# Performance work log

Hardware: AMD Instinct MI355X
Metric: run time of the kernel (lower is better)

The kernel has to match this reference:

```python
import jax, jax.numpy as jnp
import numpy as np

NUM_HEADS = 8
HEAD_DIM = 64  # inner_dim 512 / 8 heads
SCALE = HEAD_DIM ** -0.5


def setup_inputs() -> dict:
    key = jax.random.key(0)
    kq, kk, kv, kp = jax.random.split(key, 4)
    B, S, D = 8, 1024, 512
    q = jax.random.normal(kq, (B, S, D), dtype=jnp.float32)
    k = jax.random.normal(kk, (B, S, D), dtype=jnp.float32)
    v = jax.random.normal(kv, (B, S, D), dtype=jnp.float32)
    # learned additive positional bias table (trunc-normal init approximated by normal clipped)
    pos_bias = jnp.clip(jax.random.normal(kp, (1, NUM_HEADS, S, S), dtype=jnp.float32), -2.0, 2.0)
    return {"q": q, "k": k, "v": v, "pos_bias": pos_bias}


def reference(q, k, v, pos_bias):
    B, S, D = q.shape
    h, d = NUM_HEADS, HEAD_DIM
    # b n (h d) -> b h n d
    qh = q.reshape(B, S, h, d).transpose(0, 2, 1, 3) * SCALE
    kh = k.reshape(B, S, h, d).transpose(0, 2, 1, 3)
    vh = v.reshape(B, S, h, d).transpose(0, 2, 1, 3)
    sim = jnp.einsum('bhid,bhjd->bhij', qh, kh) + pos_bias
    attn = jax.nn.softmax(sim, axis=-1)
    out = jnp.einsum('bhij,bhjd->bhid', attn, vh)
    # b h n d -> b n (h d)
    return out.transpose(0, 2, 1, 3).reshape(B, S, h * d)
```

## Files before the change

### kernel.cpp

```cpp
#include <hip/hip_runtime.h>
#include <hip/hip_bf16.h>
#include <hip/hip_fp16.h>
#include <math.h>


typedef __attribute__((ext_vector_type(8))) short short8;
typedef __attribute__((ext_vector_type(4))) float f32x4;
typedef __attribute__((ext_vector_type(4))) unsigned short u16x4;
typedef __attribute__((ext_vector_type(8))) unsigned short u16x8;

#define SEQ   1024
#define DM    512
#define HD    64
#define NH    8
#define LOG2E 1.4426950408889634f
#define QSCALE (0.125f * LOG2E)

__device__ __forceinline__ unsigned short f2bf(float f) {
    unsigned u = __float_as_uint(f);
    u += 0x7fffu + ((u >> 16) & 1u);
    return (unsigned short)(u >> 16);
}
__device__ __forceinline__ u16x4 pack4(float a, float b, float c, float d) {
    u16x4 r; r[0] = f2bf(a); r[1] = f2bf(b); r[2] = f2bf(c); r[3] = f2bf(d);
    return r;
}
__device__ __forceinline__ short8 pack8(const float* x) {
    short8 r;
#pragma unroll
    for (int i = 0; i < 8; ++i) r[i] = (short)f2bf(x[i]);
    return r;
}
__device__ __forceinline__ float fexp2(float x) {
#if __has_builtin(__builtin_amdgcn_exp2f)
    return __builtin_amdgcn_exp2f(x);
#else
    return exp2f(x);
#endif
}
__device__ __forceinline__ void gll16(const void* g, void* l) {
    __builtin_amdgcn_global_load_lds(
        (const __attribute__((address_space(1))) unsigned*)g,
        (__attribute__((address_space(3))) unsigned*)l, 16, 0, 0);
}
__device__ __forceinline__ float h2f(unsigned short u) {
    __half hh = *reinterpret_cast<__half*>(&u);
    return __half2float(hh);
}
__device__ __forceinline__ unsigned short f2h(float v) {
    __half hh = __float2half(v);
    return *reinterpret_cast<unsigned short*>(&hh);
}

__global__ __launch_bounds__(256)
void prep_k(const float* __restrict__ k, short* __restrict__ kws) {
    int tid = blockIdx.x * 256 + threadIdx.x;
    int d8 = tid & 7, h = (tid >> 3) & 7, s = (tid >> 6) & 1023, b = tid >> 16;
    const float* src = k + ((size_t)(b * SEQ + s) * DM + h * HD + d8 * 8);
    float4 x0 = *(const float4*)src, x1 = *(const float4*)(src + 4);
    float xs[8] = {x0.x, x0.y, x0.z, x0.w, x1.x, x1.y, x1.z, x1.w};
    int bh = b * NH + h;
    size_t idx = (size_t)(bh * 16 + (s >> 6)) * 4096 + (s & 63) * 64 + ((d8 ^ (s & 7)) * 8);
    *(short8*)(kws + idx) = pack8(xs);
}

__global__ __launch_bounds__(256)
void prep_v(const float* __restrict__ v, short* __restrict__ vtws) {
    __shared__ short Vs[64][72];
    int bid = blockIdx.x;
    int st = bid & 15, h = (bid >> 4) & 7, b = bid >> 7;
    int t = threadIdx.x;
    {
        int sl = t >> 2, dc = t & 3;
        const float* src = v + ((size_t)(b * SEQ + st * 64 + sl) * DM + h * HD + dc * 16);
        float4 a0 = ((const float4*)src)[0], a1 = ((const float4*)src)[1],
               a2 = ((const float4*)src)[2], a3 = ((const float4*)src)[3];
        float xs0[8] = {a0.x, a0.y, a0.z, a0.w, a1.x, a1.y, a1.z, a1.w};
        float xs1[8] = {a2.x, a2.y, a2.z, a2.w, a3.x, a3.y, a3.z, a3.w};
        *(short8*)&Vs[sl][dc * 16]     = pack8(xs0);
        *(short8*)&Vs[sl][dc * 16 + 8] = pack8(xs1);
    }
    __syncthreads();
    {
        int d = t >> 2, sc = t & 3;
        short vals[16];
#pragma unroll
        for (int j = 0; j < 16; ++j) vals[j] = Vs[sc * 16 + j][d];
        short8 w0, w1;
#pragma unroll
        for (int j = 0; j < 8; ++j) { w0[j] = vals[j]; w1[j] = vals[8 + j]; }
        int bh = b * NH + h;
        size_t base = (size_t)(bh * 16 + st) * 4096 + d * 64;
        int c0 = (sc * 2) ^ (d & 7), c1 = (sc * 2 + 1) ^ (d & 7);
        *(short8*)(vtws + base + c0 * 8) = w0;
        *(short8*)(vtws + base + c1 * 8) = w1;
    }
}

__global__ __launch_bounds__(256)
void prep_bias(const float* __restrict__ bias, unsigned short* __restrict__ b16) {
    int tid = blockIdx.x * 256 + threadIdx.x;
    int h = tid >> 18;
    int rem = tid & 262143;
    int i = rem >> 8;
    int j = (rem & 255) * 4;
    float4 x = *(const float4*)(bias + ((size_t)(h * 1024 + i) * 1024 + j));
    int kt = j >> 6, jl = j & 63, mt = jl >> 4, gg = (jl >> 2) & 3;
    u16x4 r;
    r[0] = f2h(x.x * LOG2E); r[1] = f2h(x.y * LOG2E);
    r[2] = f2h(x.z * LOG2E); r[3] = f2h(x.w * LOG2E);
    *(u16x4*)(b16 + ((size_t)((h * 16 + kt) * 1024 + i) * 64 + gg * 16 + mt * 4)) = r;
}

template<int BM>
__global__ __launch_bounds__(256, 4)
void attn_fwd3(const float* __restrict__ q,
               const float* __restrict__ bias32,
               const unsigned short* __restrict__ bias16,
               const short* __restrict__ kws,
               const short* __restrict__ vtws,
               float* __restrict__ out)
{
    __shared__ short Ksh[2][4096];
    __shared__ short Vsh[2][4096];
    __shared__ short Plds[4][16][64];

    const int t = threadIdx.x;
    const int wid = t >> 6, lane = t & 63;
    const int qr = lane & 15, g = lane >> 4;

    int raw = blockIdx.x;
    int lid = (raw & 7) * 128 + (raw >> 3);
    const int b = lid & 7;
    const int h = (lid >> 3) & 7;
    const int qt = lid >> 6;
    const int qbase = qt * 64 + wid * 16;
    const int bh = b * NH + h;

    const float* qp = q + ((size_t)(b * SEQ + qbase + qr) * DM + h * HD);
    short8 qf[2];
#pragma unroll
    for (int c = 0; c < 2; ++c) {
        float4 x0 = *(const float4*)(qp + g * 8 + 32 * c);
        float4 x1 = *(const float4*)(qp + g * 8 + 32 * c + 4);
        float xs[8] = {x0.x * QSCALE, x0.y * QSCALE, x0.z * QSCALE, x0.w * QSCALE,
                       x1.x * QSCALE, x1.y * QSCALE, x1.z * QSCALE, x1.w * QSCALE};
        qf[c] = pack8(xs);
    }

    f32x4 o[4];
#pragma unroll
    for (int nt = 0; nt < 4; ++nt) o[nt] = (f32x4){0.f, 0.f, 0.f, 0.f};
    float mrun = -INFINITY, lrun = 0.f;

    const size_t tb0 = (size_t)bh * 16 * 4096;

    u16x8 bn0, bn1;
    float4 bnf[4];

    {
        const short* gk = kws + tb0 + wid * 512 + lane * 8;
        const short* gv = vtws + tb0 + wid * 512 + lane * 8;
        gll16(gk,        &Ksh[0][wid * 512]);
        gll16(gk + 2048, &Ksh[0][2048 + wid * 512]);
        gll16(gv,        &Vsh[0][wid * 512]);
        gll16(gv + 2048, &Vsh[0][2048 + wid * 512]);
        if constexpr (BM == 0) {
            const unsigned short* bp =
                bias16 + ((size_t)((h * 16 + 0) * 1024 + qbase + qr) * 64 + g * 16);
            bn0 = *(const u16x8*)bp;
            bn1 = *(const u16x8*)(bp + 8);
        } else {
            const float* bp = bias32 + ((size_t)(h * SEQ + qbase + qr) * SEQ + g * 4);
#pragma unroll
            for (int mt = 0; mt < 4; ++mt) bnf[mt] = *(const float4*)(bp + 16 * mt);
        }
    }
    __syncthreads();

    int cur = 0;
    for (int kt = 0; kt < 16; ++kt) {
        float bf[4][4];
        if constexpr (BM == 0) {
#pragma unroll
            for (int r = 0; r < 4; ++r) {
                bf[0][r] = h2f(bn0[r]);
                bf[1][r] = h2f(bn0[4 + r]);
                bf[2][r] = h2f(bn1[r]);
                bf[3][r] = h2f(bn1[4 + r]);
            }
        } else {
#pragma unroll
            for (int mt = 0; mt < 4; ++mt)
#pragma unroll
                for (int r = 0; r < 4; ++r) bf[mt][r] = ((const float*)&bnf[mt])[r];
        }

        if (kt < 15) {
            const size_t tb = tb0 + (size_t)(kt + 1) * 4096;
            const short* gk = kws + tb + wid * 512 + lane * 8;
            const short* gv = vtws + tb + wid * 512 + lane * 8;
            int nxt = cur ^ 1;
            gll16(gk,        &Ksh[nxt][wid * 512]);
            gll16(gk + 2048, &Ksh[nxt][2048 + wid * 512]);
            gll16(gv,        &Vsh[nxt][wid * 512]);
            gll16(gv + 2048, &Vsh[nxt][2048 + wid * 512]);
        }
        {
            int ktn = kt < 15 ? kt + 1 : 15;
            if constexpr (BM == 0) {
                const unsigned short* bp =
                    bias16 + ((size_t)((h * 16 + ktn) * 1024 + qbase + qr) * 64 + g * 16);
                bn0 = *(const u16x8*)bp;
                bn1 = *(const u16x8*)(bp + 8);
            } else {
                const float* bp =
                    bias32 + ((size_t)(h * SEQ + qbase + qr) * SEQ + ktn * 64 + g * 4);
#pragma unroll
                for (int mt = 0; mt < 4; ++mt) bnf[mt] = *(const float4*)(bp + 16 * mt);
            }
        }

        f32x4 acc[4];
#pragma unroll
        for (int mt = 0; mt < 4; ++mt) acc[mt] = (f32x4){0.f, 0.f, 0.f, 0.f};
        __builtin_amdgcn_s_setprio(1);
#pragma unroll
        for (int mt = 0; mt < 4; ++mt) {
#pragma unroll
            for (int c = 0; c < 2; ++c) {
                const short8 kf = *(const short8*)
                    &Ksh[cur][(qr + 16 * mt) * 64 + ((g + 4 * c) ^ (qr & 7)) * 8];
                acc[mt] = __builtin_amdgcn_mfma_f32_16x16x32_bf16(kf, qf[c], acc[mt], 0, 0, 0);
            }
        }
        __builtin_amdgcn_s_setprio(0);

        float s[4][4];
        float tmax = -INFINITY;
#pragma unroll
        for (int mt = 0; mt < 4; ++mt)
#pragma unroll
            for (int r = 0; r < 4; ++r) {
                float val;
                if constexpr (BM == 0) val = acc[mt][r] + bf[mt][r];
                else                   val = fmaf(bf[mt][r], LOG2E, acc[mt][r]);
                s[mt][r] = val;
                tmax = fmaxf(tmax, val);
            }
        tmax = fmaxf(tmax, __shfl_xor(tmax, 16));
        tmax = fmaxf(tmax, __shfl_xor(tmax, 32));
        const float mnew = fmaxf(mrun, tmax);
        float ssum = 0.f;
#pragma unroll
        for (int mt = 0; mt < 4; ++mt) {
            float e0 = fexp2(s[mt][0] - mnew);
            float e1 = fexp2(s[mt][1] - mnew);
            float e2 = fexp2(s[mt][2] - mnew);
            float e3 = fexp2(s[mt][3] - mnew);
            ssum += (e0 + e1) + (e2 + e3);
            *(u16x4*)&Plds[wid][qr][((4 * mt + g) ^ (2 * (qr & 7))) * 4] =
                pack4(e0, e1, e2, e3);
        }
        ssum += __shfl_xor(ssum, 16);
        ssum += __shfl_xor(ssum, 32);
        const float scs = fexp2(mrun - mnew);
        lrun = lrun * scs + ssum;
        mrun = mnew;

        float scr[4];
#pragma unroll
        for (int r = 0; r < 4; ++r) scr[r] = __shfl(scs, g * 4 + r);
#pragma unroll
        for (int nt = 0; nt < 4; ++nt)
#pragma unroll
            for (int r = 0; r < 4; ++r) o[nt][r] *= scr[r];

        asm volatile("s_waitcnt lgkmcnt(0)" ::: "memory");
        __builtin_amdgcn_sched_barrier(0);

        __builtin_amdgcn_s_setprio(1);
#pragma unroll
        for (int c = 0; c < 2; ++c) {
            const int ch0 = (2 * g + 8 * c) ^ (2 * (qr & 7));
            short8 pf = *(const short8*)&Plds[wid][qr][ch0 * 4];
#pragma unroll
            for (int nt = 0; nt < 4; ++nt) {
                short8 vf = *(const short8*)
                    &Vsh[cur][(qr + 16 * nt) * 64 + ((g + 4 * c) ^ (qr & 7)) * 8];
                o[nt] = __builtin_amdgcn_mfma_f32_16x16x32_bf16(pf, vf, o[nt], 0, 0, 0);
            }
        }
        __builtin_amdgcn_s_setprio(0);

        __syncthreads();
        cur ^= 1;
    }

    const float inv = 1.0f / lrun;
    float invr[4];
#pragma unroll
    for (int r = 0; r < 4; ++r) invr[r] = __shfl(inv, g * 4 + r);
    float* op = out + ((size_t)(b * SEQ + qbase) * DM + h * HD + qr);
#pragma unroll
    for (int nt = 0; nt < 4; ++nt)
#pragma unroll
        for (int r = 0; r < 4; ++r)
            op[(size_t)(g * 4 + r) * DM + nt * 16] = o[nt][r] * invr[r];
}

__global__ __launch_bounds__(256, 3)
void attn_fwd(const float* __restrict__ q, const float* __restrict__ k,
              const float* __restrict__ v, const float* __restrict__ bias,
              float* __restrict__ out)
{
    __shared__ short Klds[64][72];
    __shared__ short Vt[64][72];
    __shared__ short Pl[4][16][72];

    const int t = threadIdx.x;
    const int wid = t >> 6;
    const int lane = t & 63;
    const int qr = lane & 15;
    const int g = lane >> 4;

    int idx = blockIdx.x;
    const int b = idx & 7;  idx >>= 3;
    const int h = idx & 7;
    const int qtile = idx >> 3;
    const int qbase = qtile * 64 + wid * 16;

    const float* qp = q + ((b * SEQ + qbase + qr) * DM + h * HD);
    short8 qf[2];
#pragma unroll
    for (int c = 0; c < 2; ++c) {
        float4 x0 = *reinterpret_cast<const float4*>(qp + g * 8 + 32 * c);
        float4 x1 = *reinterpret_cast<const float4*>(qp + g * 8 + 32 * c + 4);
        float xs[8] = {x0.x * 0.125f, x0.y * 0.125f, x0.z * 0.125f, x0.w * 0.125f,
                       x1.x * 0.125f, x1.y * 0.125f, x1.z * 0.125f, x1.w * 0.125f};
        qf[c] = pack8(xs);
    }

    f32x4 o[4];
#pragma unroll
    for (int nt = 0; nt < 4; ++nt) o[nt] = (f32x4){0.f, 0.f, 0.f, 0.f};
    float mrun = -INFINITY, lrun = 0.f;

    const int jrow = t & 63;
    const int cc = t >> 6;

    for (int kt = 0; kt < 16; ++kt) {
        const int kbase = kt * 64;
        {
            const float4* kp4 = reinterpret_cast<const float4*>(
                k + ((b * SEQ + kbase + jrow) * DM + h * HD + cc * 16));
            float4 a0 = kp4[0], a1 = kp4[1], a2 = kp4[2], a3 = kp4[3];
            u16x4* dst = reinterpret_cast<u16x4*>(&Klds[jrow][cc * 16]);
            dst[0] = pack4(a0.x, a0.y, a0.z, a0.w);
            dst[1] = pack4(a1.x, a1.y, a1.z, a1.w);
            dst[2] = pack4(a2.x, a2.y, a2.z, a2.w);
            dst[3] = pack4(a3.x, a3.y, a3.z, a3.w);
        }
        {
            const float* vp = v + ((b * SEQ + kbase + cc * 16) * DM + h * HD + jrow);
            float vv[16];
#pragma unroll
            for (int jj = 0; jj < 16; ++jj) vv[jj] = vp[jj * DM];
            u16x4* dst = reinterpret_cast<u16x4*>(&Vt[jrow][cc * 16]);
            dst[0] = pack4(vv[0], vv[1], vv[2], vv[3]);
            dst[1] = pack4(vv[4], vv[5], vv[6], vv[7]);
            dst[2] = pack4(vv[8], vv[9], vv[10], vv[11]);
            dst[3] = pack4(vv[12], vv[13], vv[14], vv[15]);
        }
        __syncthreads();

        const float* bp = bias + ((h * SEQ + qbase + qr) * SEQ + kbase + g * 4);
        float4 bv0 = *reinterpret_cast<const float4*>(bp);
        float4 bv1 = *reinterpret_cast<const float4*>(bp + 16);
        float4 bv2 = *reinterpret_cast<const float4*>(bp + 32);
        float4 bv3 = *reinterpret_cast<const float4*>(bp + 48);

        f32x4 acc[4];
#pragma unroll
        for (int mt = 0; mt < 4; ++mt) {
            f32x4 a = (f32x4){0.f, 0.f, 0.f, 0.f};
#pragma unroll
            for (int c = 0; c < 2; ++c) {
                short8 kf = *reinterpret_cast<const short8*>(
                    &Klds[qr + 16 * mt][g * 8 + 32 * c]);
                a = __builtin_amdgcn_mfma_f32_16x16x32_bf16(kf, qf[c], a, 0, 0, 0);
            }
            acc[mt] = a;
        }
        acc[0][0] += bv0.x; acc[0][1] += bv0.y; acc[0][2] += bv0.z; acc[0][3] += bv0.w;
        acc[1][0] += bv1.x; acc[1][1] += bv1.y; acc[1][2] += bv1.z; acc[1][3] += bv1.w;
        acc[2][0] += bv2.x; acc[2][1] += bv2.y; acc[2][2] += bv2.z; acc[2][3] += bv2.w;
        acc[3][0] += bv3.x; acc[3][1] += bv3.y; acc[3][2] += bv3.z; acc[3][3] += bv3.w;

        float tmax = acc[0][0];
#pragma unroll
        for (int mt = 0; mt < 4; ++mt)
#pragma unroll
            for (int r = 0; r < 4; ++r) tmax = fmaxf(tmax, acc[mt][r]);
        tmax = fmaxf(tmax, __shfl_xor(tmax, 16));
        tmax = fmaxf(tmax, __shfl_xor(tmax, 32));
        const float mnew = fmaxf(mrun, tmax);

        float p[4][4];
        float ssum = 0.f;
#pragma unroll
        for (int mt = 0; mt < 4; ++mt)
#pragma unroll
            for (int r = 0; r < 4; ++r) {
                float e = __expf(acc[mt][r] - mnew);
                p[mt][r] = e;
                ssum += e;
            }
        ssum += __shfl_xor(ssum, 16);
        ssum += __shfl_xor(ssum, 32);
        const float scv = __expf(mrun - mnew);
        lrun = lrun * scv + ssum;
        mrun = mnew;

#pragma unroll
        for (int mt = 0; mt < 4; ++mt) {
            *reinterpret_cast<u16x4*>(&Pl[wid][qr][16 * mt + g * 4]) =
                pack4(p[mt][0], p[mt][1], p[mt][2], p[mt][3]);
        }

        float scr[4];
#pragma unroll
        for (int r = 0; r < 4; ++r) scr[r] = __shfl(scv, g * 4 + r);
#pragma unroll
        for (int nt = 0; nt < 4; ++nt)
#pragma unroll
            for (int r = 0; r < 4; ++r) o[nt][r] *= scr[r];

        asm volatile("s_waitcnt lgkmcnt(0)" ::: "memory");
        __builtin_amdgcn_sched_barrier(0);

        short8 pf0 = *reinterpret_cast<const short8*>(&Pl[wid][qr][g * 8]);
        short8 pf1 = *reinterpret_cast<const short8*>(&Pl[wid][qr][g * 8 + 32]);
#pragma unroll
        for (int nt = 0; nt < 4; ++nt) {
            short8 vf0 = *reinterpret_cast<const short8*>(&Vt[qr + 16 * nt][g * 8]);
            short8 vf1 = *reinterpret_cast<const short8*>(&Vt[qr + 16 * nt][g * 8 + 32]);
            o[nt] = __builtin_amdgcn_mfma_f32_16x16x32_bf16(pf0, vf0, o[nt], 0, 0, 0);
            o[nt] = __builtin_amdgcn_mfma_f32_16x16x32_bf16(pf1, vf1, o[nt], 0, 0, 0);
        }
        __syncthreads();
    }

    const float inv = 1.0f / lrun;
    float invr[4];
#pragma unroll
    for (int r = 0; r < 4; ++r) invr[r] = __shfl(inv, g * 4 + r);

    float* op = out + ((b * SEQ + qbase) * DM + h * HD + qr);
#pragma unroll
    for (int nt = 0; nt < 4; ++nt)
#pragma unroll
        for (int r = 0; r < 4; ++r)
            op[(g * 4 + r) * DM + nt * 16] = o[nt][r] * invr[r];
}

extern "C" void kernel_launch(void* const* d_in, const int* in_sizes, int n_in,
                              void* d_out, int out_size, void* d_ws, size_t ws_size,
                              hipStream_t stream) {
    const float* q    = (const float*)d_in[0];
    const float* k    = (const float*)d_in[1];
    const float* v    = (const float*)d_in[2];
    const float* bias = (const float*)d_in[3];
    float* out        = (float*)d_out;

    const size_t kv_elems  = (size_t)8 * NH * SEQ * HD;
    const size_t kv_bytes  = 2 * kv_elems * sizeof(short);
    const size_t b16_bytes = (size_t)NH * SEQ * SEQ * 2;

    if (ws_size >= b16_bytes + kv_bytes) {
        unsigned short* b16 = (unsigned short*)d_ws;
        short* kws  = (short*)((char*)d_ws + b16_bytes);
        short* vtws = kws + kv_elems;
        prep_bias<<<dim3(8192), dim3(256), 0, stream>>>(bias, b16);
        prep_k<<<dim3(2048), dim3(256), 0, stream>>>(k, kws);
        prep_v<<<dim3(1024), dim3(256), 0, stream>>>(v, vtws);
        attn_fwd3<0><<<dim3(1024), dim3(256), 0, stream>>>(q, nullptr, b16, kws, vtws, out);
    } else if (ws_size >= kv_bytes) {
        short* kws  = (short*)d_ws;
        short* vtws = kws + kv_elems;
        prep_k<<<dim3(2048), dim3(256), 0, stream>>>(k, kws);
        prep_v<<<dim3(1024), dim3(256), 0, stream>>>(v, vtws);
        attn_fwd3<1><<<dim3(1024), dim3(256), 0, stream>>>(q, bias, nullptr, kws, vtws, out);
    } else {
        attn_fwd<<<dim3(1024), dim3(256), 0, stream>>>(q, k, v, bias, out);
    }
}
```

Before: 163.8 us.

## Fuse prep kernels, pass P via ds_bpermute, add lazy softmax rescale

Merges the three preprocessing kernels into a single launch, which removes two kernel launch gaps. In the attention kernel, the P tile is no longer staged through LDS: it is packed into registers and redistributed across lanes with ds_bpermute. The running-max rescale of the output accumulators is skipped unless a wave's new max exceeds the old one by a threshold. The occupancy hint is raised from 4 to 5 blocks. The lazy rescale lets exp2 values reach up to 2^8, which risks precision loss in bf16 P, and the extra bpermutes and selects add VALU work.

After: 160.2 us. 1.02x faster.

```diff
diff --git a/kernel.cpp b/kernel.cpp
--- a/kernel.cpp
+++ b/kernel.cpp
@@ -15,6 +15,7 @@
 #define NH    8
 #define LOG2E 1.4426950408889634f
 #define QSCALE (0.125f * LOG2E)
+#define RESCALE_THR 8.0f
 
 __device__ __forceinline__ unsigned short f2bf(float f) {
     unsigned u = __float_as_uint(f);
@@ -53,67 +54,69 @@
 }
 
 __global__ __launch_bounds__(256)
-void prep_k(const float* __restrict__ k, short* __restrict__ kws) {
-    int tid = blockIdx.x * 256 + threadIdx.x;
-    int d8 = tid & 7, h = (tid >> 3) & 7, s = (tid >> 6) & 1023, b = tid >> 16;
-    const float* src = k + ((size_t)(b * SEQ + s) * DM + h * HD + d8 * 8);
-    float4 x0 = *(const float4*)src, x1 = *(const float4*)(src + 4);
-    float xs[8] = {x0.x, x0.y, x0.z, x0.w, x1.x, x1.y, x1.z, x1.w};
-    int bh = b * NH + h;
-    size_t idx = (size_t)(bh * 16 + (s >> 6)) * 4096 + (s & 63) * 64 + ((d8 ^ (s & 7)) * 8);
-    *(short8*)(kws + idx) = pack8(xs);
-}
-
-__global__ __launch_bounds__(256)
-void prep_v(const float* __restrict__ v, short* __restrict__ vtws) {
-    __shared__ short Vs[64][72];
-    int bid = blockIdx.x;
-    int st = bid & 15, h = (bid >> 4) & 7, b = bid >> 7;
-    int t = threadIdx.x;
-    {
-        int sl = t >> 2, dc = t & 3;
-        const float* src = v + ((size_t)(b * SEQ + st * 64 + sl) * DM + h * HD + dc * 16);
-        float4 a0 = ((const float4*)src)[0], a1 = ((const float4*)src)[1],
-               a2 = ((const float4*)src)[2], a3 = ((const float4*)src)[3];
-        float xs0[8] = {a0.x, a0.y, a0.z, a0.w, a1.x, a1.y, a1.z, a1.w};
-        float xs1[8] = {a2.x, a2.y, a2.z, a2.w, a3.x, a3.y, a3.z, a3.w};
-        *(short8*)&Vs[sl][dc * 16]     = pack8(xs0);
-        *(short8*)&Vs[sl][dc * 16 + 8] = pack8(xs1);
-    }
-    __syncthreads();
-    {
-        int d = t >> 2, sc = t & 3;
-        short vals[16];
-#pragma unroll
-        for (int j = 0; j < 16; ++j) vals[j] = Vs[sc * 16 + j][d];
-        short8 w0, w1;
-#pragma unroll
-        for (int j = 0; j < 8; ++j) { w0[j] = vals[j]; w1[j] = vals[8 + j]; }
+void prep_all(const float* __restrict__ k, const float* __restrict__ v,
+              const float* __restrict__ bias,
+              short* __restrict__ kws, short* __restrict__ vtws,
+              unsigned short* __restrict__ b16)
+{
+    const int bid = blockIdx.x;
+    const int t = threadIdx.x;
+    if (bid < 8192) {
+        if (b16 == nullptr) return;
+        int tid = bid * 256 + t;
+        int h = tid >> 18;
+        int rem = tid & 262143;
+        int i = rem >> 8;
+        int j = (rem & 255) * 4;
+        float4 x = *(const float4*)(bias + ((size_t)(h * 1024 + i) * 1024 + j));
+        int kt = j >> 6, jl = j & 63, mt = jl >> 4, gg = (jl >> 2) & 3;
+        u16x4 r;
+        r[0] = f2h(x.x * LOG2E); r[1] = f2h(x.y * LOG2E);
+        r[2] = f2h(x.z * LOG2E); r[3] = f2h(x.w * LOG2E);
+        *(u16x4*)(b16 + ((size_t)((h * 16 + kt) * 1024 + i) * 64 + gg * 16 + mt * 4)) = r;
+    } else if (bid < 8192 + 2048) {
+        int tid = (bid - 8192) * 256 + t;
+        int d8 = tid & 7, h = (tid >> 3) & 7, s = (tid >> 6) & 1023, b = tid >> 16;
+        const float* src = k + ((size_t)(b * SEQ + s) * DM + h * HD + d8 * 8);
+        float4 x0 = *(const float4*)src, x1 = *(const float4*)(src + 4);
+        float xs[8] = {x0.x, x0.y, x0.z, x0.w, x1.x, x1.y, x1.z, x1.w};
         int bh = b * NH + h;
-        size_t base = (size_t)(bh * 16 + st) * 4096 + d * 64;
-        int c0 = (sc * 2) ^ (d & 7), c1 = (sc * 2 + 1) ^ (d & 7);
-        *(short8*)(vtws + base + c0 * 8) = w0;
-        *(short8*)(vtws + base + c1 * 8) = w1;
-    }
-}
-
-__global__ __launch_bounds__(256)
-void prep_bias(const float* __restrict__ bias, unsigned short* __restrict__ b16) {
-    int tid = blockIdx.x * 256 + threadIdx.x;
-    int h = tid >> 18;
-    int rem = tid & 262143;
-    int i = rem >> 8;
-    int j = (rem & 255) * 4;
-    float4 x = *(const float4*)(bias + ((size_t)(h * 1024 + i) * 1024 + j));
-    int kt = j >> 6, jl = j & 63, mt = jl >> 4, gg = (jl >> 2) & 3;
-    u16x4 r;
-    r[0] = f2h(x.x * LOG2E); r[1] = f2h(x.y * LOG2E);
-    r[2] = f2h(x.z * LOG2E); r[3] = f2h(x.w * LOG2E);
-    *(u16x4*)(b16 + ((size_t)((h * 16 + kt) * 1024 + i) * 64 + gg * 16 + mt * 4)) = r;
+        size_t idx = (size_t)(bh * 16 + (s >> 6)) * 4096 + (s & 63) * 64 + ((d8 ^ (s & 7)) * 8);
+        *(short8*)(kws + idx) = pack8(xs);
+    } else {
+        __shared__ short Vs[64][72];
+        int bid3 = bid - 10240;
+        int st = bid3 & 15, h = (bid3 >> 4) & 7, b = bid3 >> 7;
+        {
+            int sl = t >> 2, dc = t & 3;
+            const float* src = v + ((size_t)(b * SEQ + st * 64 + sl) * DM + h * HD + dc * 16);
+            float4 a0 = ((const float4*)src)[0], a1 = ((const float4*)src)[1],
+                   a2 = ((const float4*)src)[2], a3 = ((const float4*)src)[3];
+            float xs0[8] = {a0.x, a0.y, a0.z, a0.w, a1.x, a1.y, a1.z, a1.w};
+            float xs1[8] = {a2.x, a2.y, a2.z, a2.w, a3.x, a3.y, a3.z, a3.w};
+            *(short8*)&Vs[sl][dc * 16]     = pack8(xs0);
+            *(short8*)&Vs[sl][dc * 16 + 8] = pack8(xs1);
+        }
+        __syncthreads();
+        {
+            int d = t >> 2, sc = t & 3;
+            short vals[16];
+#pragma unroll
+            for (int j = 0; j < 16; ++j) vals[j] = Vs[sc * 16 + j][d];
+            short8 w0, w1;
+#pragma unroll
+            for (int j = 0; j < 8; ++j) { w0[j] = vals[j]; w1[j] = vals[8 + j]; }
+            int bh = b * NH + h;
+            size_t base = (size_t)(bh * 16 + st) * 4096 + d * 64;
+            int c0 = (sc * 2) ^ (d & 7), c1 = (sc * 2 + 1) ^ (d & 7);
+            *(short8*)(vtws + base + c0 * 8) = w0;
+            *(short8*)(vtws + base + c1 * 8) = w1;
+        }
+    }
 }
 
 template<int BM>
-__global__ __launch_bounds__(256, 4)
+__global__ __launch_bounds__(256, 5)
 void attn_fwd3(const float* __restrict__ q,
                const float* __restrict__ bias32,
                const unsigned short* __restrict__ bias16,
@@ -123,7 +126,6 @@
 {
     __shared__ short Ksh[2][4096];
     __shared__ short Vsh[2][4096];
-    __shared__ short Plds[4][16][64];
 
     const int t = threadIdx.x;
     const int wid = t >> 6, lane = t & 63;
@@ -136,6 +138,10 @@
     const int qt = lid >> 6;
     const int qbase = qt * 64 + wid * 16;
     const int bh = b * NH + h;
+
+    const int srcA = (qr + 32 * (g & 1)) << 2;
+    const int srcB = srcA + 64;
+    const bool hi = (g >> 1) != 0;
 
     const float* qp = q + ((size_t)(b * SEQ + qbase + qr) * DM + h * HD);
     short8 qf[2];
@@ -250,48 +256,62 @@
             }
         tmax = fmaxf(tmax, __shfl_xor(tmax, 16));
         tmax = fmaxf(tmax, __shfl_xor(tmax, 32));
-        const float mnew = fmaxf(mrun, tmax);
+
+        if (!__all(tmax <= mrun + RESCALE_THR)) {
+            const float mnew = fmaxf(mrun, tmax);
+            const float scs = fexp2(mrun - mnew);
+            float scr[4];
+#pragma unroll
+            for (int r = 0; r < 4; ++r) scr[r] = __shfl(scs, g * 4 + r);
+#pragma unroll
+            for (int nt = 0; nt < 4; ++nt)
+#pragma unroll
+                for (int r = 0; r < 4; ++r) o[nt][r] *= scr[r];
+            lrun *= scs;
+            mrun = mnew;
+        }
+
         float ssum = 0.f;
+        unsigned W[4][2];
 #pragma unroll
         for (int mt = 0; mt < 4; ++mt) {
-            float e0 = fexp2(s[mt][0] - mnew);
-            float e1 = fexp2(s[mt][1] - mnew);
-            float e2 = fexp2(s[mt][2] - mnew);
-            float e3 = fexp2(s[mt][3] - mnew);
+            float e0 = fexp2(s[mt][0] - mrun);
+            float e1 = fexp2(s[mt][1] - mrun);
+            float e2 = fexp2(s[mt][2] - mrun);
+            float e3 = fexp2(s[mt][3] - mrun);
             ssum += (e0 + e1) + (e2 + e3);
-            *(u16x4*)&Plds[wid][qr][((4 * mt + g) ^ (2 * (qr & 7))) * 4] =
-                pack4(e0, e1, e2, e3);
+            W[mt][0] = (unsigned)f2bf(e0) | ((unsigned)f2bf(e1) << 16);
+            W[mt][1] = (unsigned)f2bf(e2) | ((unsigned)f2bf(e3) << 16);
         }
         ssum += __shfl_xor(ssum, 16);
         ssum += __shfl_xor(ssum, 32);
-        const float scs = fexp2(mrun - mnew);
-        lrun = lrun * scs + ssum;
-        mrun = mnew;
-
-        float scr[4];
-#pragma unroll
-        for (int r = 0; r < 4; ++r) scr[r] = __shfl(scs, g * 4 + r);
-#pragma unroll
-        for (int nt = 0; nt < 4; ++nt)
-#pragma unroll
-            for (int r = 0; r < 4; ++r) o[nt][r] *= scr[r];
-
-        asm volatile("s_waitcnt lgkmcnt(0)" ::: "memory");
-        __builtin_amdgcn_sched_barrier(0);
-
-        __builtin_amdgcn_s_setprio(1);
+        lrun += ssum;
+
 #pragma unroll
         for (int c = 0; c < 2; ++c) {
-            const int ch0 = (2 * g + 8 * c) ^ (2 * (qr & 7));
-            short8 pf = *(const short8*)&Plds[wid][qr][ch0 * 4];
+            unsigned Ra[2][2], Rb[2][2];
+#pragma unroll
+            for (int mo = 0; mo < 2; ++mo)
+#pragma unroll
+                for (int w = 0; w < 2; ++w) {
+                    Ra[mo][w] = (unsigned)__builtin_amdgcn_ds_bpermute(srcA, (int)W[2 * c + mo][w]);
+                    Rb[mo][w] = (unsigned)__builtin_amdgcn_ds_bpermute(srcB, (int)W[2 * c + mo][w]);
+                }
+            union { unsigned u[4]; short8 s8; } P_;
+            P_.u[0] = hi ? Ra[1][0] : Ra[0][0];
+            P_.u[1] = hi ? Ra[1][1] : Ra[0][1];
+            P_.u[2] = hi ? Rb[1][0] : Rb[0][0];
+            P_.u[3] = hi ? Rb[1][1] : Rb[0][1];
+            const short8 pf = P_.s8;
+            __builtin_amdgcn_s_setprio(1);
 #pragma unroll
             for (int nt = 0; nt < 4; ++nt) {
                 short8 vf = *(const short8*)
                     &Vsh[cur][(qr + 16 * nt) * 64 + ((g + 4 * c) ^ (qr & 7)) * 8];
                 o[nt] = __builtin_amdgcn_mfma_f32_16x16x32_bf16(pf, vf, o[nt], 0, 0, 0);
             }
-        }
-        __builtin_amdgcn_s_setprio(0);
+            __builtin_amdgcn_s_setprio(0);
+        }
 
         __syncthreads();
         cur ^= 1;
@@ -481,15 +501,12 @@
         unsigned short* b16 = (unsigned short*)d_ws;
         short* kws  = (short*)((char*)d_ws + b16_bytes);
         short* vtws = kws + kv_elems;
-        prep_bias<<<dim3(8192), dim3(256), 0, stream>>>(bias, b16);
-        prep_k<<<dim3(2048), dim3(256), 0, stream>>>(k, kws);
-        prep_v<<<dim3(1024), dim3(256), 0, stream>>>(v, vtws);
+        prep_all<<<dim3(11264), dim3(256), 0, stream>>>(k, v, bias, kws, vtws, b16);
         attn_fwd3<0><<<dim3(1024), dim3(256), 0, stream>>>(q, nullptr, b16, kws, vtws, out);
     } else if (ws_size >= kv_bytes) {
         short* kws  = (short*)d_ws;
         short* vtws = kws + kv_elems;
-        prep_k<<<dim3(2048), dim3(256), 0, stream>>>(k, kws);
-        prep_v<<<dim3(1024), dim3(256), 0, stream>>>(v, vtws);
+        prep_all<<<dim3(11264), dim3(256), 0, stream>>>(k, v, bias, kws, vtws, nullptr);
         attn_fwd3<1><<<dim3(1024), dim3(256), 0, stream>>>(q, bias, nullptr, kws, vtws, out);
     } else {
         attn_fwd<<<dim3(1024), dim3(256), 0, stream>>>(q, k, v, bias, out);
```
